# Kernel optimization log

Hardware: AMD Instinct MI355X
Metric: run time of the kernel (lower is better)

Reference implementation:

```python
import jax, jax.numpy as jnp
import numpy as np

B, N, D = 32, 2048, 1024


def setup_inputs() -> dict:
    key0 = jax.random.key(0)
    ks = jax.random.split(key0, 9)
    scale = 1.0 / np.sqrt(D)
    query = jax.random.normal(ks[0], (B, D), dtype=jnp.float32)
    key = jax.random.normal(ks[1], (B, N, D), dtype=jnp.float32)
    mask = jax.random.randint(ks[2], (B, N), 0, 2, dtype=jnp.int32)
    W1 = jax.random.uniform(ks[3], (D, D), jnp.float32, -scale, scale)
    b1 = jax.random.uniform(ks[4], (D,), jnp.float32, -scale, scale)
    W2 = jax.random.uniform(ks[5], (D, D), jnp.float32, -scale, scale)
    b2 = jax.random.uniform(ks[6], (D,), jnp.float32, -scale, scale)
    v_w = jax.random.uniform(ks[7], (D,), jnp.float32, -scale, scale)
    v_b = jax.random.uniform(ks[8], (), jnp.float32, -scale, scale)
    return {"query": query, "key": key, "mask": mask,
            "W1": W1, "b1": b1, "W2": W2, "b2": b2, "v_w": v_w, "v_b": v_b}


def reference(query, key, mask, W1, b1, W2, b2, v_w, v_b):
    # key_out: [B, N, D] = key @ W1^T + b1 (nn.Linear convention)
    key_out = jnp.einsum('bnd,ed->bne', key, W1) + b1
    # query_out: [B, D] -> broadcast over N
    query_out = jnp.einsum('bd,ed->be', query, W2) + b2
    h = jnp.tanh(key_out + query_out[:, None, :])  # [B, N, D]
    ui = jnp.einsum('bnd,d->bn', h, v_w) + v_b      # v: D -> 1, squeezed
    ui = jnp.where(mask.astype(bool), ui, -jnp.inf)
    return ui
```

## Files before the change

kernel.cpp:

```cpp
#include <hip/hip_runtime.h>
#include <hip/hip_bf16.h>
#include <math.h>

#define B_ 32
#define N_ 2048
#define D_ 1024
#define M_ (B_ * N_)

typedef float  fx4  __attribute__((ext_vector_type(4)));
typedef __bf16 bf16x8 __attribute__((ext_vector_type(8)));
typedef unsigned short us4 __attribute__((ext_vector_type(4)));

#define WS_W1B   134217728ULL
#define WS_T     136314880ULL
#define WS_ACC   136445952ULL

#define MASK_NEG_SENTINEL (-1.0e30f)

__device__ inline unsigned short f2b(float f) {
    __hip_bfloat16 h = __float2bfloat16(f);
    return *reinterpret_cast<unsigned short*>(&h);
}

__global__ void key_convert_kernel(const fx4* __restrict__ key4,
                                   us4* __restrict__ keyb4) {
    const int total = 16777216;
    int idx    = blockIdx.x * blockDim.x + threadIdx.x;
    int stride = gridDim.x * blockDim.x;
    for (int i = idx; i < total; i += stride) {
        fx4 v = key4[i];
        us4 o; o.x = f2b(v.x); o.y = f2b(v.y); o.z = f2b(v.z); o.w = f2b(v.w);
        keyb4[i] = o;
    }
}

__global__ void w1_convert_kernel(const fx4* __restrict__ W1,
                                  us4* __restrict__ w1b4) {
    int idx = blockIdx.x * blockDim.x + threadIdx.x;
#pragma unroll
    for (int i = 0; i < 4; ++i) {
        int j = idx + i * 65536;
        fx4 v = W1[j];
        us4 o; o.x = f2b(v.x); o.y = f2b(v.y); o.z = f2b(v.z); o.w = f2b(v.w);
        w1b4[j] = o;
    }
}

__global__ void tq_kernel(const float* __restrict__ query,
                          const float* __restrict__ W2,
                          const float* __restrict__ b1,
                          const float* __restrict__ b2,
                          float* __restrict__ t) {
    int tid = threadIdx.x;
    int p = blockIdx.x * 32 + (tid >> 3);
    int j = tid & 7;
    int b = p >> 10;
    int e = p & 1023;
    const fx4* q = (const fx4*)query + (size_t)b * 256;
    const fx4* w = (const fx4*)W2 + (size_t)e * 256;
    float acc = 0.f;
#pragma unroll 4
    for (int it = 0; it < 32; ++it) {
        int k4 = it * 8 + j;
        fx4 qv = q[k4];
        fx4 wv = w[k4];
        acc += qv.x * wv.x + qv.y * wv.y + qv.z * wv.z + qv.w * wv.w;
    }
    acc += __shfl_xor(acc, 1);
    acc += __shfl_xor(acc, 2);
    acc += __shfl_xor(acc, 4);
    if (j == 0) t[p] = acc + b1[e] + b2[e];
}

__device__ inline float fast_tanh(float x) {
    float ax = fabsf(x);
    float e  = __expf(-2.0f * ax);
    float r  = (1.0f - e) / (1.0f + e);
    return copysignf(r, x);
}

#define BM 128
#define BN 128
#define BK 32

#define GLD16(g, l)                                                        \
    __builtin_amdgcn_global_load_lds(                                      \
        (const __attribute__((address_space(1))) void*)(g),                \
        (__attribute__((address_space(3))) void*)(l), 16, 0, 0)

__global__ void __launch_bounds__(256)
main_gemm(const unsigned short* __restrict__ keyb,
          const unsigned short* __restrict__ w1b,
          const float* __restrict__ t,
          const float* __restrict__ v_w,
          float* __restrict__ accum) {
    __shared__ unsigned short As[BM * BK];
    __shared__ unsigned short Bs[BN * BK];

    const int tid  = threadIdx.x;
    const int lane = tid & 63;
    const int wave = tid >> 6;
    const int quad = lane >> 4;
    const int l15  = lane & 15;
    const int m0 = blockIdx.y * BM;
    const int e0 = blockIdx.x * BN;
    const int mw = (wave >> 1) * 64;
    const int ew = (wave & 1) * 64;

    const int srow  = tid >> 2;
    const int skoff = (tid & 3) * 8;
    const unsigned short* aSrc0 = keyb + (size_t)(m0 + srow) * D_ + skoff;
    const unsigned short* aSrc1 = aSrc0 + (size_t)64 * D_;
    const unsigned short* bSrc0 = w1b + (size_t)(e0 + srow) * D_ + skoff;
    const unsigned short* bSrc1 = bSrc0 + (size_t)64 * D_;
    char* AsB = (char*)As;
    char* BsB = (char*)Bs;
    char* aDst0 = AsB + wave * 1024;
    char* aDst1 = AsB + 4096 + wave * 1024;
    char* bDst0 = BsB + wave * 1024;
    char* bDst1 = BsB + 4096 + wave * 1024;

    fx4 acc[4][4] = {};

    for (int k0 = 0; k0 < D_; k0 += BK) {
        GLD16(aSrc0 + k0, aDst0);
        GLD16(aSrc1 + k0, aDst1);
        GLD16(bSrc0 + k0, bDst0);
        GLD16(bSrc1 + k0, bDst1);
        __syncthreads();

        bf16x8 a[4], b[4];
#pragma unroll
        for (int i = 0; i < 4; ++i) {
            int ml = mw + i * 16 + l15;
            a[i] = *(const bf16x8*)(&As[ml * BK + quad * 8]);
        }
#pragma unroll
        for (int j = 0; j < 4; ++j) {
            int el = ew + j * 16 + l15;
            b[j] = *(const bf16x8*)(&Bs[el * BK + quad * 8]);
        }
#pragma unroll
        for (int i = 0; i < 4; ++i)
#pragma unroll
            for (int j = 0; j < 4; ++j)
                acc[i][j] = __builtin_amdgcn_mfma_f32_16x16x32_bf16(
                    a[i], b[j], acc[i][j], 0, 0, 0);

        __syncthreads();
    }

    const float* trow = t + (size_t)(m0 >> 11) * D_;
    float vwv[4], tqv[4];
#pragma unroll
    for (int j = 0; j < 4; ++j) {
        int e = e0 + ew + j * 16 + l15;
        vwv[j] = v_w[e];
        tqv[j] = trow[e];
    }
#pragma unroll
    for (int i = 0; i < 4; ++i) {
#pragma unroll
        for (int r = 0; r < 4; ++r) {
            float s = 0.f;
#pragma unroll
            for (int j = 0; j < 4; ++j)
                s += vwv[j] * fast_tanh(acc[i][j][r] + tqv[j]);
            s += __shfl_xor(s, 1);
            s += __shfl_xor(s, 2);
            s += __shfl_xor(s, 4);
            s += __shfl_xor(s, 8);
            if (l15 == 0) {
                int m = m0 + mw + i * 16 + quad * 4 + r;
                atomicAdd(&accum[m], s);
            }
        }
    }
}

__global__ void finalize_kernel(const float* __restrict__ accum,
                                const int* __restrict__ mask,
                                const float* __restrict__ v_b,
                                float* __restrict__ out) {
    int i = blockIdx.x * blockDim.x + threadIdx.x;
    if (i < M_) {
        float vb = v_b[0];
        out[i] = mask[i] ? (accum[i] + vb) : MASK_NEG_SENTINEL;
    }
}

extern "C" void kernel_launch(void* const* d_in, const int* in_sizes, int n_in,
                              void* d_out, int out_size, void* d_ws, size_t ws_size,
                              hipStream_t stream) {
    const float* query = (const float*)d_in[0];
    const float* key   = (const float*)d_in[1];
    const int*   mask  = (const int*)d_in[2];
    const float* W1    = (const float*)d_in[3];
    const float* b1    = (const float*)d_in[4];
    const float* W2    = (const float*)d_in[5];
    const float* b2    = (const float*)d_in[6];
    const float* v_w   = (const float*)d_in[7];
    const float* v_b   = (const float*)d_in[8];

    char* ws = (char*)d_ws;
    unsigned short* keyb = (unsigned short*)ws;
    unsigned short* w1b  = (unsigned short*)(ws + WS_W1B);
    float*          t    = (float*)(ws + WS_T);
    float*          acc  = (float*)(ws + WS_ACC);

    key_convert_kernel<<<4096, 256, 0, stream>>>((const fx4*)key, (us4*)keyb);
    w1_convert_kernel<<<256, 256, 0, stream>>>((const fx4*)W1, (us4*)w1b);
    tq_kernel<<<1024, 256, 0, stream>>>(query, W2, b1, b2, t);
    hipMemsetAsync(acc, 0, (size_t)M_ * sizeof(float), stream);
    dim3 g(8, 512);
    main_gemm<<<g, 256, 0, stream>>>(keyb, w1b, t, v_w, acc);
    finalize_kernel<<<M_ / 256, 256, 0, stream>>>(acc, mask, v_b, (float*)d_out);
}
```

Measured before the change: 611.2 us.

## Fuse key bf16 conversion, GEMM, tanh-reduce and masking into one kernel

Drops the separate pass that converts key to bf16, the memset, the atomics and the finalize kernel. Each 512-thread block now loads a 64-row fp32 key tile, converts it into a 128 KB swizzled LDS buffer, and loops over every output column. Each wave streams its slice of bf16 W1 straight from global/L2 and reduces across waves through shared memory before writing masked outputs. This saves the key bf16 write and re-read and the atomic traffic, but one block per CU and W1 fragments loaded directly from global with no LDS staging could starve the MFMA units.

```diff
diff --git a/kernel.cpp b/kernel.cpp
--- a/kernel.cpp
+++ b/kernel.cpp
@@ -10,28 +10,15 @@
 typedef float  fx4  __attribute__((ext_vector_type(4)));
 typedef __bf16 bf16x8 __attribute__((ext_vector_type(8)));
 typedef unsigned short us4 __attribute__((ext_vector_type(4)));
-
-#define WS_W1B   134217728ULL
-#define WS_T     136314880ULL
-#define WS_ACC   136445952ULL
+typedef unsigned short us8 __attribute__((ext_vector_type(8)));
+
+#define WS_T 2097152ULL
 
 #define MASK_NEG_SENTINEL (-1.0e30f)
 
 __device__ inline unsigned short f2b(float f) {
     __hip_bfloat16 h = __float2bfloat16(f);
     return *reinterpret_cast<unsigned short*>(&h);
-}
-
-__global__ void key_convert_kernel(const fx4* __restrict__ key4,
-                                   us4* __restrict__ keyb4) {
-    const int total = 16777216;
-    int idx    = blockIdx.x * blockDim.x + threadIdx.x;
-    int stride = gridDim.x * blockDim.x;
-    for (int i = idx; i < total; i += stride) {
-        fx4 v = key4[i];
-        us4 o; o.x = f2b(v.x); o.y = f2b(v.y); o.z = f2b(v.z); o.w = f2b(v.w);
-        keyb4[i] = o;
-    }
 }
 
 __global__ void w1_convert_kernel(const fx4* __restrict__ W1,
@@ -79,113 +66,117 @@
     return copysignf(r, x);
 }
 
-#define BM 128
-#define BN 128
-#define BK 32
-
-#define GLD16(g, l)                                                        \
-    __builtin_amdgcn_global_load_lds(                                      \
-        (const __attribute__((address_space(1))) void*)(g),                \
-        (__attribute__((address_space(3))) void*)(l), 16, 0, 0)
-
-__global__ void __launch_bounds__(256)
-main_gemm(const unsigned short* __restrict__ keyb,
-          const unsigned short* __restrict__ w1b,
-          const float* __restrict__ t,
-          const float* __restrict__ v_w,
-          float* __restrict__ accum) {
-    __shared__ unsigned short As[BM * BK];
-    __shared__ unsigned short Bs[BN * BK];
+#define BM 64
+#define WNC 64
+#define NCHUNK 2
+
+__global__ void __launch_bounds__(512)
+fused_main(const float* __restrict__ key,
+           const unsigned short* __restrict__ w1b,
+           const float* __restrict__ t,
+           const float* __restrict__ v_w,
+           const float* __restrict__ v_b,
+           const int* __restrict__ mask,
+           float* __restrict__ out) {
+    __shared__ unsigned short As[BM * D_];
+    __shared__ float rs[8][BM];
 
     const int tid  = threadIdx.x;
     const int lane = tid & 63;
     const int wave = tid >> 6;
     const int quad = lane >> 4;
     const int l15  = lane & 15;
-    const int m0 = blockIdx.y * BM;
-    const int e0 = blockIdx.x * BN;
-    const int mw = (wave >> 1) * 64;
-    const int ew = (wave & 1) * 64;
-
-    const int srow  = tid >> 2;
-    const int skoff = (tid & 3) * 8;
-    const unsigned short* aSrc0 = keyb + (size_t)(m0 + srow) * D_ + skoff;
-    const unsigned short* aSrc1 = aSrc0 + (size_t)64 * D_;
-    const unsigned short* bSrc0 = w1b + (size_t)(e0 + srow) * D_ + skoff;
-    const unsigned short* bSrc1 = bSrc0 + (size_t)64 * D_;
-    char* AsB = (char*)As;
-    char* BsB = (char*)Bs;
-    char* aDst0 = AsB + wave * 1024;
-    char* aDst1 = AsB + 4096 + wave * 1024;
-    char* bDst0 = BsB + wave * 1024;
-    char* bDst1 = BsB + 4096 + wave * 1024;
-
-    fx4 acc[4][4] = {};
-
-    for (int k0 = 0; k0 < D_; k0 += BK) {
-        GLD16(aSrc0 + k0, aDst0);
-        GLD16(aSrc1 + k0, aDst1);
-        GLD16(bSrc0 + k0, bDst0);
-        GLD16(bSrc1 + k0, bDst1);
-        __syncthreads();
-
-        bf16x8 a[4], b[4];
-#pragma unroll
-        for (int i = 0; i < 4; ++i) {
-            int ml = mw + i * 16 + l15;
-            a[i] = *(const bf16x8*)(&As[ml * BK + quad * 8]);
-        }
+    const int m0   = blockIdx.x * BM;
+
+    {
+#pragma unroll
+        for (int r8 = 0; r8 < 8; ++r8) {
+            const int row = wave * 8 + r8;
+            const fx4* src = (const fx4*)(key + (size_t)(m0 + row) * D_);
+#pragma unroll
+            for (int p = 0; p < 2; ++p) {
+                const int s = p * 64 + lane;
+                fx4 v0 = src[s * 2];
+                fx4 v1 = src[s * 2 + 1];
+                us8 o;
+                o[0] = f2b(v0.x); o[1] = f2b(v0.y);
+                o[2] = f2b(v0.z); o[3] = f2b(v0.w);
+                o[4] = f2b(v1.x); o[5] = f2b(v1.y);
+                o[6] = f2b(v1.z); o[7] = f2b(v1.w);
+                const int ss = s ^ (row & 7);
+                *(us8*)((char*)As + row * 2048 + ss * 16) = o;
+            }
+        }
+    }
+    __syncthreads();
+
+    const int b_idx = m0 >> 11;
+    const float* trow = t + (size_t)b_idx * D_;
+    float rsum[4][4] = {};
+
+    for (int c = 0; c < NCHUNK; ++c) {
+        const int e0 = wave * (WNC * NCHUNK) + c * WNC;
+        fx4 acc[4][4] = {};
+        const unsigned short* bptr =
+            w1b + (size_t)(e0 + l15) * D_ + quad * 8;
+
+        for (int k0 = 0; k0 < D_; k0 += 32) {
+            bf16x8 a[4], b[4];
+#pragma unroll
+            for (int j = 0; j < 4; ++j)
+                b[j] = *(const bf16x8*)(bptr + (size_t)j * 16 * D_ + k0);
+#pragma unroll
+            for (int i = 0; i < 4; ++i) {
+                const int row  = i * 16 + l15;
+                const int slot = ((k0 >> 3) + quad) ^ (row & 7);
+                a[i] = *(const bf16x8*)((const char*)As + row * 2048 + slot * 16);
+            }
+#pragma unroll
+            for (int i = 0; i < 4; ++i)
+#pragma unroll
+                for (int j = 0; j < 4; ++j)
+                    acc[i][j] = __builtin_amdgcn_mfma_f32_16x16x32_bf16(
+                        a[i], b[j], acc[i][j], 0, 0, 0);
+        }
+
+        float vwv[4], tqv[4];
 #pragma unroll
         for (int j = 0; j < 4; ++j) {
-            int el = ew + j * 16 + l15;
-            b[j] = *(const bf16x8*)(&Bs[el * BK + quad * 8]);
+            const int e = e0 + j * 16 + l15;
+            vwv[j] = v_w[e];
+            tqv[j] = trow[e];
         }
 #pragma unroll
         for (int i = 0; i < 4; ++i)
 #pragma unroll
-            for (int j = 0; j < 4; ++j)
-                acc[i][j] = __builtin_amdgcn_mfma_f32_16x16x32_bf16(
-                    a[i], b[j], acc[i][j], 0, 0, 0);
-
-        __syncthreads();
-    }
-
-    const float* trow = t + (size_t)(m0 >> 11) * D_;
-    float vwv[4], tqv[4];
-#pragma unroll
-    for (int j = 0; j < 4; ++j) {
-        int e = e0 + ew + j * 16 + l15;
-        vwv[j] = v_w[e];
-        tqv[j] = trow[e];
-    }
-#pragma unroll
-    for (int i = 0; i < 4; ++i) {
+            for (int r = 0; r < 4; ++r) {
+                float s = 0.f;
+#pragma unroll
+                for (int j = 0; j < 4; ++j)
+                    s += vwv[j] * fast_tanh(acc[i][j][r] + tqv[j]);
+                rsum[i][r] += s;
+            }
+    }
+
+#pragma unroll
+    for (int i = 0; i < 4; ++i)
 #pragma unroll
         for (int r = 0; r < 4; ++r) {
-            float s = 0.f;
-#pragma unroll
-            for (int j = 0; j < 4; ++j)
-                s += vwv[j] * fast_tanh(acc[i][j][r] + tqv[j]);
+            float s = rsum[i][r];
             s += __shfl_xor(s, 1);
             s += __shfl_xor(s, 2);
             s += __shfl_xor(s, 4);
             s += __shfl_xor(s, 8);
-            if (l15 == 0) {
-                int m = m0 + mw + i * 16 + quad * 4 + r;
-                atomicAdd(&accum[m], s);
-            }
-        }
-    }
-}
-
-__global__ void finalize_kernel(const float* __restrict__ accum,
-                                const int* __restrict__ mask,
-                                const float* __restrict__ v_b,
-                                float* __restrict__ out) {
-    int i = blockIdx.x * blockDim.x + threadIdx.x;
-    if (i < M_) {
-        float vb = v_b[0];
-        out[i] = mask[i] ? (accum[i] + vb) : MASK_NEG_SENTINEL;
+            if (l15 == 0) rs[wave][i * 16 + quad * 4 + r] = s;
+        }
+    __syncthreads();
+
+    if (tid < BM) {
+        float u = 0.f;
+#pragma unroll
+        for (int w = 0; w < 8; ++w) u += rs[w][tid];
+        const int m = m0 + tid;
+        out[m] = mask[m] ? (u + v_b[0]) : MASK_NEG_SENTINEL;
     }
 }
 
@@ -203,16 +194,11 @@
     const float* v_b   = (const float*)d_in[8];
 
     char* ws = (char*)d_ws;
-    unsigned short* keyb = (unsigned short*)ws;
-    unsigned short* w1b  = (unsigned short*)(ws + WS_W1B);
-    float*          t    = (float*)(ws + WS_T);
-    float*          acc  = (float*)(ws + WS_ACC);
-
-    key_convert_kernel<<<4096, 256, 0, stream>>>((const fx4*)key, (us4*)keyb);
+    unsigned short* w1b = (unsigned short*)ws;
+    float*          t   = (float*)(ws + WS_T);
+
     w1_convert_kernel<<<256, 256, 0, stream>>>((const fx4*)W1, (us4*)w1b);
     tq_kernel<<<1024, 256, 0, stream>>>(query, W2, b1, b2, t);
-    hipMemsetAsync(acc, 0, (size_t)M_ * sizeof(float), stream);
-    dim3 g(8, 512);
-    main_gemm<<<g, 256, 0, stream>>>(keyb, w1b, t, v_w, acc);
-    finalize_kernel<<<M_ / 256, 256, 0, stream>>>(acc, mask, v_b, (float*)d_out);
-}
+    fused_main<<<M_ / BM, 512, 0, stream>>>(key, w1b, t, v_w, v_b, mask,
+                                            (float*)d_out);
+}
```

After: 627.2 us. 2.6% more time.

## Pre-swizzle bf16 operands into tile-contiguous layout and fuse prep kernels

Applied to the files above, without the earlier changes.

The conversion kernels now write key and W1 as bf16 in a pre-tiled, XOR-swizzled layout. Each GEMM k-step then loads a contiguous 8KB chunk, and the LDS reads avoid bank conflicts. The key/W1 conversion, the query projection and the accumulator zeroing are merged into one prep kernel, which removes several launches and the memset. The GEMM grid is remapped to a 1D order that groups M tiles for better L2 reuse of W1 tiles. The cost is a more complex indexing scheme that must match exactly between the producer and the consumer.

```diff
diff --git a/kernel.cpp b/kernel.cpp
--- a/kernel.cpp
+++ b/kernel.cpp
@@ -10,66 +10,96 @@
 typedef float  fx4  __attribute__((ext_vector_type(4)));
 typedef __bf16 bf16x8 __attribute__((ext_vector_type(8)));
 typedef unsigned short us4 __attribute__((ext_vector_type(4)));
-
-#define WS_W1B   134217728ULL
-#define WS_T     136314880ULL
-#define WS_ACC   136445952ULL
+typedef unsigned short us8 __attribute__((ext_vector_type(8)));
+
+#define WS_W1S 134217728ULL
+#define WS_T   136314880ULL
+#define WS_ACC 136445952ULL
 
 #define MASK_NEG_SENTINEL (-1.0e30f)
+
 
 __device__ inline unsigned short f2b(float f) {
     __hip_bfloat16 h = __float2bfloat16(f);
     return *reinterpret_cast<unsigned short*>(&h);
 }
 
-__global__ void key_convert_kernel(const fx4* __restrict__ key4,
-                                   us4* __restrict__ keyb4) {
-    const int total = 16777216;
-    int idx    = blockIdx.x * blockDim.x + threadIdx.x;
-    int stride = gridDim.x * blockDim.x;
-    for (int i = idx; i < total; i += stride) {
-        fx4 v = key4[i];
-        us4 o; o.x = f2b(v.x); o.y = f2b(v.y); o.z = f2b(v.z); o.w = f2b(v.w);
-        keyb4[i] = o;
-    }
-}
-
-__global__ void w1_convert_kernel(const fx4* __restrict__ W1,
-                                  us4* __restrict__ w1b4) {
-    int idx = blockIdx.x * blockDim.x + threadIdx.x;
-#pragma unroll
-    for (int i = 0; i < 4; ++i) {
-        int j = idx + i * 65536;
-        fx4 v = W1[j];
-        us4 o; o.x = f2b(v.x); o.y = f2b(v.y); o.z = f2b(v.z); o.w = f2b(v.w);
-        w1b4[j] = o;
-    }
-}
-
-__global__ void tq_kernel(const float* __restrict__ query,
-                          const float* __restrict__ W2,
-                          const float* __restrict__ b1,
-                          const float* __restrict__ b2,
-                          float* __restrict__ t) {
-    int tid = threadIdx.x;
-    int p = blockIdx.x * 32 + (tid >> 3);
-    int j = tid & 7;
-    int b = p >> 10;
-    int e = p & 1023;
-    const fx4* q = (const fx4*)query + (size_t)b * 256;
-    const fx4* w = (const fx4*)W2 + (size_t)e * 256;
-    float acc = 0.f;
+__global__ void prep_kernel(const float* __restrict__ key,
+                            char* __restrict__ keyS,
+                            const float* __restrict__ W1,
+                            char* __restrict__ w1S,
+                            const float* __restrict__ query,
+                            const float* __restrict__ W2,
+                            const float* __restrict__ b1,
+                            const float* __restrict__ b2,
+                            float* __restrict__ t,
+                            fx4* __restrict__ accz) {
+    const int bid = blockIdx.x;
+    const int tid = threadIdx.x;
+    if (bid < 1024) {
+        int u = bid * 256 + tid;
+        int row = u >> 2, q = u & 3;
+        const fx4* src = (const fx4*)(key + (size_t)row * D_) + q * 2;
+        int r = row & 127;
+        int sphys = (((r & 1) << 2) | q) ^ ((r >> 1) & 7);
+        int tphys = ((r & 63) >> 1) * 8 + sphys;
+        char* dst = keyS + (size_t)(row >> 7) * 262144
+                  + ((r >> 6) & 1) * 4096 + tphys * 16;
 #pragma unroll 4
-    for (int it = 0; it < 32; ++it) {
-        int k4 = it * 8 + j;
-        fx4 qv = q[k4];
-        fx4 wv = w[k4];
-        acc += qv.x * wv.x + qv.y * wv.y + qv.z * wv.z + qv.w * wv.w;
-    }
-    acc += __shfl_xor(acc, 1);
-    acc += __shfl_xor(acc, 2);
-    acc += __shfl_xor(acc, 4);
-    if (j == 0) t[p] = acc + b1[e] + b2[e];
+        for (int k = 0; k < 32; ++k) {
+            fx4 v0 = src[k * 8];
+            fx4 v1 = src[k * 8 + 1];
+            us8 o;
+            o[0] = f2b(v0.x); o[1] = f2b(v0.y);
+            o[2] = f2b(v0.z); o[3] = f2b(v0.w);
+            o[4] = f2b(v1.x); o[5] = f2b(v1.y);
+            o[6] = f2b(v1.z); o[7] = f2b(v1.w);
+            *(us8*)(dst + (size_t)k * 8192) = o;
+        }
+    } else if (bid < 1040) {
+        int u = (bid - 1024) * 256 + tid;
+        int e = u >> 2, q = u & 3;
+        const fx4* src = (const fx4*)(W1 + (size_t)e * D_) + q * 2;
+        int r = e & 127;
+        int sphys = (((r & 1) << 2) | q) ^ ((r >> 1) & 7);
+        int tphys = ((r & 63) >> 1) * 8 + sphys;
+        char* dst = w1S + (size_t)(e >> 7) * 262144
+                  + ((r >> 6) & 1) * 4096 + tphys * 16;
+#pragma unroll 4
+        for (int k = 0; k < 32; ++k) {
+            fx4 v0 = src[k * 8];
+            fx4 v1 = src[k * 8 + 1];
+            us8 o;
+            o[0] = f2b(v0.x); o[1] = f2b(v0.y);
+            o[2] = f2b(v0.z); o[3] = f2b(v0.w);
+            o[4] = f2b(v1.x); o[5] = f2b(v1.y);
+            o[6] = f2b(v1.z); o[7] = f2b(v1.w);
+            *(us8*)(dst + (size_t)k * 8192) = o;
+        }
+    } else if (bid < 2064) {
+        int p = (bid - 1040) * 32 + (tid >> 3);
+        int j = tid & 7;
+        int b = p >> 10;
+        int e = p & 1023;
+        const fx4* q = (const fx4*)query + (size_t)b * 256;
+        const fx4* w = (const fx4*)W2 + (size_t)e * 256;
+        float acc = 0.f;
+#pragma unroll 4
+        for (int it = 0; it < 32; ++it) {
+            int k4 = it * 8 + j;
+            fx4 qv = q[k4];
+            fx4 wv = w[k4];
+            acc += qv.x * wv.x + qv.y * wv.y + qv.z * wv.z + qv.w * wv.w;
+        }
+        acc += __shfl_xor(acc, 1);
+        acc += __shfl_xor(acc, 2);
+        acc += __shfl_xor(acc, 4);
+        if (j == 0) t[p] = acc + b1[e] + b2[e];
+    } else {
+        int idx = (bid - 2064) * 256 + tid;
+        fx4 z = {0.f, 0.f, 0.f, 0.f};
+        accz[idx] = z;
+    }
 }
 
 __device__ inline float fast_tanh(float x) {
@@ -79,67 +109,71 @@
     return copysignf(r, x);
 }
 
-#define BM 128
-#define BN 128
-#define BK 32
-
 #define GLD16(g, l)                                                        \
     __builtin_amdgcn_global_load_lds(                                      \
         (const __attribute__((address_space(1))) void*)(g),                \
         (__attribute__((address_space(3))) void*)(l), 16, 0, 0)
 
 __global__ void __launch_bounds__(256)
-main_gemm(const unsigned short* __restrict__ keyb,
-          const unsigned short* __restrict__ w1b,
+main_gemm(const char* __restrict__ keyS,
+          const char* __restrict__ w1S,
           const float* __restrict__ t,
           const float* __restrict__ v_w,
           float* __restrict__ accum) {
-    __shared__ unsigned short As[BM * BK];
-    __shared__ unsigned short Bs[BN * BK];
+    __shared__ char As[8192];
+    __shared__ char Bs[8192];
 
     const int tid  = threadIdx.x;
     const int lane = tid & 63;
     const int wave = tid >> 6;
     const int quad = lane >> 4;
     const int l15  = lane & 15;
-    const int m0 = blockIdx.y * BM;
-    const int e0 = blockIdx.x * BN;
+
+    const int p_ = blockIdx.x;
+    const int mt = (p_ >> 6) * 8 + (p_ & 7);
+    const int et = (p_ >> 3) & 7;
+    const int m0 = mt * 128;
+    const int e0 = et * 128;
     const int mw = (wave >> 1) * 64;
     const int ew = (wave & 1) * 64;
 
-    const int srow  = tid >> 2;
-    const int skoff = (tid & 3) * 8;
-    const unsigned short* aSrc0 = keyb + (size_t)(m0 + srow) * D_ + skoff;
-    const unsigned short* aSrc1 = aSrc0 + (size_t)64 * D_;
-    const unsigned short* bSrc0 = w1b + (size_t)(e0 + srow) * D_ + skoff;
-    const unsigned short* bSrc1 = bSrc0 + (size_t)64 * D_;
-    char* AsB = (char*)As;
-    char* BsB = (char*)Bs;
-    char* aDst0 = AsB + wave * 1024;
-    char* aDst1 = AsB + 4096 + wave * 1024;
-    char* bDst0 = BsB + wave * 1024;
-    char* bDst1 = BsB + 4096 + wave * 1024;
+    const char* aB = keyS + (size_t)mt * 262144 + tid * 16;
+    const char* bB = w1S + (size_t)et * 262144 + tid * 16;
+    char* aD = (char*)As + wave * 1024;
+    char* bD = (char*)Bs + wave * 1024;
+
+    int aOff[4], bOff[4];
+#pragma unroll
+    for (int i = 0; i < 4; ++i) {
+        int row = mw + i * 16 + l15;
+        aOff[i] = (row >> 1) * 128 +
+                  ((((row & 1) << 2) | quad) ^ ((row >> 1) & 7)) * 16;
+    }
+#pragma unroll
+    for (int j = 0; j < 4; ++j) {
+        int el = ew + j * 16 + l15;
+        bOff[j] = (el >> 1) * 128 +
+                  ((((el & 1) << 2) | quad) ^ ((el >> 1) & 7)) * 16;
+    }
 
     fx4 acc[4][4] = {};
 
-    for (int k0 = 0; k0 < D_; k0 += BK) {
-        GLD16(aSrc0 + k0, aDst0);
-        GLD16(aSrc1 + k0, aDst1);
-        GLD16(bSrc0 + k0, bDst0);
-        GLD16(bSrc1 + k0, bDst1);
+    for (int k = 0; k < 32; ++k) {
+        const char* ak = aB + (size_t)k * 8192;
+        const char* bk = bB + (size_t)k * 8192;
+        GLD16(ak, aD);
+        GLD16(ak + 4096, aD + 4096);
+        GLD16(bk, bD);
+        GLD16(bk + 4096, bD + 4096);
         __syncthreads();
 
         bf16x8 a[4], b[4];
 #pragma unroll
-        for (int i = 0; i < 4; ++i) {
-            int ml = mw + i * 16 + l15;
-            a[i] = *(const bf16x8*)(&As[ml * BK + quad * 8]);
-        }
-#pragma unroll
-        for (int j = 0; j < 4; ++j) {
-            int el = ew + j * 16 + l15;
-            b[j] = *(const bf16x8*)(&Bs[el * BK + quad * 8]);
-        }
+        for (int i = 0; i < 4; ++i)
+            a[i] = *(const bf16x8*)((const char*)As + aOff[i]);
+#pragma unroll
+        for (int j = 0; j < 4; ++j)
+            b[j] = *(const bf16x8*)((const char*)Bs + bOff[j]);
 #pragma unroll
         for (int i = 0; i < 4; ++i)
 #pragma unroll
@@ -203,16 +237,14 @@
     const float* v_b   = (const float*)d_in[8];
 
     char* ws = (char*)d_ws;
-    unsigned short* keyb = (unsigned short*)ws;
-    unsigned short* w1b  = (unsigned short*)(ws + WS_W1B);
-    float*          t    = (float*)(ws + WS_T);
-    float*          acc  = (float*)(ws + WS_ACC);
-
-    key_convert_kernel<<<4096, 256, 0, stream>>>((const fx4*)key, (us4*)keyb);
-    w1_convert_kernel<<<256, 256, 0, stream>>>((const fx4*)W1, (us4*)w1b);
-    tq_kernel<<<1024, 256, 0, stream>>>(query, W2, b1, b2, t);
-    hipMemsetAsync(acc, 0, (size_t)M_ * sizeof(float), stream);
-    dim3 g(8, 512);
-    main_gemm<<<g, 256, 0, stream>>>(keyb, w1b, t, v_w, acc);
-    finalize_kernel<<<M_ / 256, 256, 0, stream>>>(acc, mask, v_b, (float*)d_out);
-}
+    char*  keyS = ws;
+    char*  w1S  = ws + WS_W1S;
+    float* t    = (float*)(ws + WS_T);
+    float* acc  = (float*)(ws + WS_ACC);
+
+    prep_kernel<<<2128, 256, 0, stream>>>(key, keyS, W1, w1S,
+                                          query, W2, b1, b2, t, (fx4*)acc);
+    main_gemm<<<4096, 256, 0, stream>>>(keyS, w1S, t, v_w, acc);
+    finalize_kernel<<<M_ / 256, 256, 0, stream>>>(acc, mask, v_b,
+                                                  (float*)d_out);
+}
```

Measured after the change: 578.7 us. 5.3% less time.
